# Optimization experiments

Hardware: AMD Instinct MI355X
Metric: run time of the kernel (lower is better)

The kernel has to match this reference:

```python
import jax, jax.numpy as jnp
import numpy as np

ROPE_BASE = 10000.0

def _rope_cos_sin(seq_len, head_dim, dtype):
    half = head_dim // 2
    inv_freq = 1.0 / (ROPE_BASE ** (jnp.arange(0, half, dtype=jnp.float32) / half))
    ang = jnp.arange(seq_len, dtype=jnp.float32)[:, None] * inv_freq[None, :]  # [S, half]
    ang = jnp.concatenate([ang, ang], axis=-1)  # [S, D]
    return jnp.cos(ang).astype(dtype), jnp.sin(ang).astype(dtype)

def _rotate_half(t):
    d = t.shape[-1] // 2
    return jnp.concatenate([-t[..., d:], t[..., :d]], axis=-1)

def _apply_rope(t, cos, sin):
    # t: [B, H, S, D]; cos/sin: [S, D]
    return t * cos[None, None, :, :] + _rotate_half(t) * sin[None, None, :, :]

def setup_inputs() -> dict:
    key = jax.random.key(0)
    ks = jax.random.split(key, 6)
    B, S, DM = 2, 2048, 2048
    x = jax.random.normal(ks[0], (B, S, DM), dtype=jnp.float32)
    attention_mask = jnp.ones((B, S), dtype=jnp.bool_)
    scale = 1.0 / np.sqrt(DM)
    W_in = jax.random.normal(ks[1], (DM, 3 * DM), dtype=jnp.float32) * scale
    b_in = jax.random.normal(ks[2], (3 * DM,), dtype=jnp.float32) * 0.02
    W_out = jax.random.normal(ks[3], (DM, DM), dtype=jnp.float32) * scale
    b_out = jax.random.normal(ks[4], (DM,), dtype=jnp.float32) * 0.02
    return {"x": x, "attention_mask": attention_mask, "W_in": W_in,
            "b_in": b_in, "W_out": W_out, "b_out": b_out}

def reference(x, attention_mask, W_in, b_in, W_out, b_out):
    B, S, DM = x.shape
    H = 16
    D = DM // H
    qkv = x @ W_in + b_in                         # [B, S, 3*DM]
    q, k, v = jnp.split(qkv, 3, axis=-1)
    def to_heads(t):
        return t.reshape(B, S, H, D).transpose(0, 2, 1, 3)  # [B, H, S, D]
    q, k, v = to_heads(q), to_heads(k), to_heads(v)
    cos, sin = _rope_cos_sin(S, D, x.dtype)
    q = _apply_rope(q, cos, sin)
    k = _apply_rope(k, cos, sin)
    scale = 1.0 / np.sqrt(D).astype(np.float32)
    scores = jnp.einsum('bhqd,bhkd->bhqk', q, k) * scale   # [B, H, S, S]
    # SDPA bool mask semantics: True = attend, False = mask out
    mask = attention_mask[:, None, None, :]
    scores = jnp.where(mask, scores, jnp.finfo(scores.dtype).min)
    attn = jax.nn.softmax(scores, axis=-1)
    out = jnp.einsum('bhqk,bhkd->bhqd', attn, v)           # [B, H, S, D]
    out = out.transpose(0, 2, 1, 3).reshape(B, S, DM)
    return out @ W_out + b_out
```

## Files before the change

### kernel.cpp

```cpp
#include <hip/hip_runtime.h>
#include <math.h>

typedef _Float16 f16;
typedef _Float16 f16x4 __attribute__((ext_vector_type(4)));
typedef _Float16 f16x8 __attribute__((ext_vector_type(8)));
typedef float    f32x4 __attribute__((ext_vector_type(4)));

__device__ __forceinline__ void lds_async16(void* lds, const void* g) {
  __builtin_amdgcn_global_load_lds(
      (const __attribute__((address_space(1))) void*)g,
      (__attribute__((address_space(3))) void*)lds, 16, 0, 0);
}

__device__ __forceinline__ f16x4 shfl8(f16x4 v, int srcLane) {
  union { f16x4 h; int i[2]; } u;
  u.h = v;
  u.i[0] = __shfl(u.i[0], srcLane, 64);
  u.i[1] = __shfl(u.i[1], srcLane, 64);
  return u.h;
}

#define BARRIER_FENCE() do { __builtin_amdgcn_s_barrier(); asm volatile("" ::: "memory"); } while (0)
#define WAIT_LGKM0()    asm volatile("s_waitcnt lgkmcnt(0)" ::: "memory")


__global__ __launch_bounds__(256) void f2h4_kernel(const float* __restrict__ in,
                                                   f16* __restrict__ out, int n4) {
  int i = blockIdx.x * 256 + threadIdx.x;
  if (i < n4) {
    float4 v = ((const float4*)in)[i];
    f16x4 h;
    h.x = (f16)v.x; h.y = (f16)v.y; h.z = (f16)v.z; h.w = (f16)v.w;
    ((f16x4*)out)[i] = h;
  }
}

__global__ __launch_bounds__(256) void transpose_f2h(const float* __restrict__ in,
                                                     f16* __restrict__ out,
                                                     int rows, int cols) {
  __shared__ f16 t[64][65];
  int r0 = blockIdx.x * 64, c0 = blockIdx.y * 64;
  int tid = threadIdx.x;
#pragma unroll
  for (int i = 0; i < 16; ++i) {
    int idx = i * 256 + tid;
    int r = idx >> 6, c = idx & 63;
    t[r][c] = (f16)in[(size_t)(r0 + r) * cols + c0 + c];
  }
  __syncthreads();
#pragma unroll
  for (int i = 0; i < 16; ++i) {
    int idx = i * 256 + tid;
    int c = idx >> 6, r = idx & 63;
    out[(size_t)(c0 + c) * rows + r0 + r] = t[r][c];
  }
}

__global__ __launch_bounds__(256) void rope_table_k(float* __restrict__ cosT,
                                                    float* __restrict__ sinT) {
  int idx = blockIdx.x * 256 + threadIdx.x;
  int s = idx >> 6, j = idx & 63;
  double invf = pow(10000.0, -(double)j / 64.0);
  double a = fmod((double)s * invf, 6.283185307179586476925287);
  cosT[s * 64 + j] = (float)cos(a);
  sinT[s * 64 + j] = (float)sin(a);
}

__global__ __launch_bounds__(512, 4) void gemm_qkv(const f16* __restrict__ A,
                                                   const f16* __restrict__ Bt,
                                                   const float* __restrict__ bias,
                                                   const float* __restrict__ cosT,
                                                   const float* __restrict__ sinT,
                                                   f16* __restrict__ Qh, f16* __restrict__ Kh,
                                                   f16* __restrict__ Vt) {
  const int Kd = 2048;
  __shared__ __align__(16) f16 smem[32768];
  f16* Asb = smem;
  f16* Bsb = smem + 16384;
  int tid = threadIdx.x;
  int lane = tid & 63, wave = tid >> 6;
  int wm = wave >> 2, wn = wave & 3;
  int l15 = lane & 15, l4 = lane >> 4;
  int bn = blockIdx.x * 128, bm = blockIdx.y * 128;

  auto stageAq = [&](int buf, int kt, int qh) {
    int rl = tid >> 3, gl = tid & 7;
    int row = qh * 32 + (rl & 31) + (rl >> 5) * 64;
    int gg = gl ^ (rl & 7);
    lds_async16(&Asb[buf * 8192 + row * 64 + gl * 8],
                A + (size_t)(bm + row) * Kd + kt * 64 + gg * 8);
  };
  auto stageBh = [&](int buf, int kt, int h) {
    int rl = tid >> 3, gl = tid & 7;
    int row = h * 64 + rl;
    int gg = gl ^ (rl & 7);
    lds_async16(&Bsb[buf * 8192 + row * 64 + gl * 8],
                Bt + (size_t)(bn + row) * Kd + kt * 64 + gg * 8);
  };

  f32x4 acc[4][2] = {};

  stageAq(0, 0, 0); stageAq(0, 0, 1); stageBh(0, 0, 0); stageBh(0, 0, 1);
  stageAq(1, 1, 0); stageBh(1, 1, 0);
  asm volatile("s_waitcnt vmcnt(2)" ::: "memory");
  BARRIER_FENCE();

  for (int t = 0; t < 32; ++t) {
    int cb = t & 1;
    const f16* as = Asb + cb * 8192;
    const f16* bs = Bsb + cb * 8192;
    f16x8 af[2], bf[2];

#pragma unroll
    for (int j = 0; j < 2; ++j)
      af[j] = *(const f16x8*)&as[(wm * 64 + j * 16 + l15) * 64 + ((l4 ^ (l15 & 7)) * 8)];
#pragma unroll
    for (int nf = 0; nf < 2; ++nf)
      bf[nf] = *(const f16x8*)&bs[((wn + nf * 4) * 16 + l15) * 64 + ((l4 ^ (l15 & 7)) * 8)];
    if (t + 1 < 32) { stageAq(cb ^ 1, t + 1, 1); stageBh(cb ^ 1, t + 1, 1); }
    BARRIER_FENCE();
    WAIT_LGKM0();
    __builtin_amdgcn_s_setprio(1);
#pragma unroll
    for (int j = 0; j < 2; ++j)
#pragma unroll
      for (int nf = 0; nf < 2; ++nf)
        acc[j][nf] = __builtin_amdgcn_mfma_f32_16x16x32_f16(af[j], bf[nf], acc[j][nf], 0, 0, 0);
    __builtin_amdgcn_s_setprio(0);
    BARRIER_FENCE();

#pragma unroll
    for (int j = 0; j < 2; ++j)
      af[j] = *(const f16x8*)&as[(wm * 64 + (2 + j) * 16 + l15) * 64 + ((l4 ^ (l15 & 7)) * 8)];
    BARRIER_FENCE();
    WAIT_LGKM0();
    __builtin_amdgcn_s_setprio(1);
#pragma unroll
    for (int j = 0; j < 2; ++j)
#pragma unroll
      for (int nf = 0; nf < 2; ++nf)
        acc[2 + j][nf] = __builtin_amdgcn_mfma_f32_16x16x32_f16(af[j], bf[nf], acc[2 + j][nf], 0, 0, 0);
    __builtin_amdgcn_s_setprio(0);
    BARRIER_FENCE();

#pragma unroll
    for (int j = 0; j < 2; ++j)
      af[j] = *(const f16x8*)&as[(wm * 64 + j * 16 + l15) * 64 + (((4 + l4) ^ (l15 & 7)) * 8)];
#pragma unroll
    for (int nf = 0; nf < 2; ++nf)
      bf[nf] = *(const f16x8*)&bs[((wn + nf * 4) * 16 + l15) * 64 + (((4 + l4) ^ (l15 & 7)) * 8)];
    BARRIER_FENCE();
    WAIT_LGKM0();
    __builtin_amdgcn_s_setprio(1);
#pragma unroll
    for (int j = 0; j < 2; ++j)
#pragma unroll
      for (int nf = 0; nf < 2; ++nf)
        acc[j][nf] = __builtin_amdgcn_mfma_f32_16x16x32_f16(af[j], bf[nf], acc[j][nf], 0, 0, 0);
    __builtin_amdgcn_s_setprio(0);
    BARRIER_FENCE();

#pragma unroll
    for (int j = 0; j < 2; ++j)
      af[j] = *(const f16x8*)&as[(wm * 64 + (2 + j) * 16 + l15) * 64 + (((4 + l4) ^ (l15 & 7)) * 8)];
    if (t + 2 < 32) { stageBh(cb, t + 2, 0); stageAq(cb, t + 2, 0); }
    BARRIER_FENCE();
    WAIT_LGKM0();
    __builtin_amdgcn_s_setprio(1);
#pragma unroll
    for (int j = 0; j < 2; ++j)
#pragma unroll
      for (int nf = 0; nf < 2; ++nf)
        acc[2 + j][nf] = __builtin_amdgcn_mfma_f32_16x16x32_f16(af[j], bf[nf], acc[2 + j][nf], 0, 0, 0);
    __builtin_amdgcn_s_setprio(0);
    if (t < 30) asm volatile("s_waitcnt vmcnt(2)" ::: "memory");
    else        asm volatile("s_waitcnt vmcnt(0)" ::: "memory");
    BARRIER_FENCE();
  }

  int which = bn >> 11;
  int head  = (bn & 2047) >> 7;
  if (which < 2) {
    f16* dst = which == 0 ? Qh : Kh;
    const float qsc = which == 0 ? 0.08838834764831845f : 1.0f;
    int dlo = wn * 16 + l15;
#pragma unroll
    for (int mi = 0; mi < 4; ++mi)
#pragma unroll
      for (int r = 0; r < 4; ++r) {
        int gm = bm + wm * 64 + mi * 16 + l4 * 4 + r;
        int b = gm >> 11, s = gm & 2047;
        size_t rowbase = ((size_t)(b * 16 + head) * 2048 + s) << 7;
        float cth = cosT[s * 64 + dlo], sth = sinT[s * 64 + dlo];
        float lo = acc[mi][0][r] + bias[bn + dlo];
        float hi = acc[mi][1][r] + bias[bn + dlo + 64];
        dst[rowbase + dlo]      = (f16)((lo * cth - hi * sth) * qsc);
        dst[rowbase + dlo + 64] = (f16)((hi * cth + lo * sth) * qsc);
      }
  } else {
    __syncthreads();
    f16* Vsc = smem;
#pragma unroll
    for (int mi = 0; mi < 4; ++mi)
#pragma unroll
      for (int nf = 0; nf < 2; ++nf) {
        int d = (wn + nf * 4) * 16 + l15;
        int s = wm * 64 + mi * 16 + l4 * 4;
        f16x4 v;
#pragma unroll
        for (int r = 0; r < 4; ++r) v[r] = (f16)(acc[mi][nf][r] + bias[bn + d]);
        int off = d * 128 + ((((s >> 3) ^ ((d & 7) << 1))) << 3) + (s & 7);
        *(f16x4*)&Vsc[off] = v;
      }
    __syncthreads();
    int bm2 = bm & 2047, b = bm >> 11;
#pragma unroll
    for (int it = 0; it < 4; ++it) {
      int idx = it * 512 + tid;
      int d = idx >> 4, gs = idx & 15;
      f16x8 v = *(const f16x8*)&Vsc[d * 128 + ((gs ^ ((d & 7) << 1)) << 3)];
      *(f16x8*)&Vt[((size_t)(b * 16 + head) * 128 + d) * 2048 + bm2 + gs * 8] = v;
    }
  }
}

__global__ __launch_bounds__(512, 4) void gemm_out(const f16* __restrict__ A,
                                                   const f16* __restrict__ Bt,
                                                   const float* __restrict__ bias,
                                                   float* __restrict__ C) {
  const int Kd = 2048, Nd = 2048;
  __shared__ __align__(16) f16 smem[32768];
  f16* Asb = smem;
  f16* Bsb = smem + 16384;
  int tid = threadIdx.x;
  int lane = tid & 63, wave = tid >> 6;
  int wm = wave >> 2, wn = wave & 3;
  int l15 = lane & 15, l4 = lane >> 4;
  int bm = blockIdx.x * 128, bn = blockIdx.y * 128;

  auto stageAq = [&](int buf, int kt, int qh) {
    int rl = tid >> 3, gl = tid & 7;
    int row = qh * 32 + (rl & 31) + (rl >> 5) * 64;
    int gg = gl ^ (rl & 7);
    lds_async16(&Asb[buf * 8192 + row * 64 + gl * 8],
                A + (size_t)(bm + row) * Kd + kt * 64 + gg * 8);
  };
  auto stageBh = [&](int buf, int kt, int h) {
    int rl = tid >> 3, gl = tid & 7;
    int row = h * 64 + rl;
    int gg = gl ^ (rl & 7);
    lds_async16(&Bsb[buf * 8192 + row * 64 + gl * 8],
                Bt + (size_t)(bn + row) * Kd + kt * 64 + gg * 8);
  };

  f32x4 acc[4][2] = {};

  stageAq(0, 0, 0); stageAq(0, 0, 1); stageBh(0, 0, 0); stageBh(0, 0, 1);
  stageAq(1, 1, 0); stageBh(1, 1, 0);
  asm volatile("s_waitcnt vmcnt(2)" ::: "memory");
  BARRIER_FENCE();

  for (int t = 0; t < 32; ++t) {
    int cb = t & 1;
    const f16* as = Asb + cb * 8192;
    const f16* bs = Bsb + cb * 8192;
    f16x8 af[2], bf[2];

#pragma unroll
    for (int j = 0; j < 2; ++j)
      af[j] = *(const f16x8*)&as[(wm * 64 + j * 16 + l15) * 64 + ((l4 ^ (l15 & 7)) * 8)];
#pragma unroll
    for (int nf = 0; nf < 2; ++nf)
      bf[nf] = *(const f16x8*)&bs[(wn * 32 + nf * 16 + l15) * 64 + ((l4 ^ (l15 & 7)) * 8)];
    if (t + 1 < 32) { stageAq(cb ^ 1, t + 1, 1); stageBh(cb ^ 1, t + 1, 1); }
    BARRIER_FENCE();
    WAIT_LGKM0();
    __builtin_amdgcn_s_setprio(1);
#pragma unroll
    for (int j = 0; j < 2; ++j)
#pragma unroll
      for (int nf = 0; nf < 2; ++nf)
        acc[j][nf] = __builtin_amdgcn_mfma_f32_16x16x32_f16(af[j], bf[nf], acc[j][nf], 0, 0, 0);
    __builtin_amdgcn_s_setprio(0);
    BARRIER_FENCE();

#pragma unroll
    for (int j = 0; j < 2; ++j)
      af[j] = *(const f16x8*)&as[(wm * 64 + (2 + j) * 16 + l15) * 64 + ((l4 ^ (l15 & 7)) * 8)];
    BARRIER_FENCE();
    WAIT_LGKM0();
    __builtin_amdgcn_s_setprio(1);
#pragma unroll
    for (int j = 0; j < 2; ++j)
#pragma unroll
      for (int nf = 0; nf < 2; ++nf)
        acc[2 + j][nf] = __builtin_amdgcn_mfma_f32_16x16x32_f16(af[j], bf[nf], acc[2 + j][nf], 0, 0, 0);
    __builtin_amdgcn_s_setprio(0);
    BARRIER_FENCE();

#pragma unroll
    for (int j = 0; j < 2; ++j)
      af[j] = *(const f16x8*)&as[(wm * 64 + j * 16 + l15) * 64 + (((4 + l4) ^ (l15 & 7)) * 8)];
#pragma unroll
    for (int nf = 0; nf < 2; ++nf)
      bf[nf] = *(const f16x8*)&bs[(wn * 32 + nf * 16 + l15) * 64 + (((4 + l4) ^ (l15 & 7)) * 8)];
    BARRIER_FENCE();
    WAIT_LGKM0();
    __builtin_amdgcn_s_setprio(1);
#pragma unroll
    for (int j = 0; j < 2; ++j)
#pragma unroll
      for (int nf = 0; nf < 2; ++nf)
        acc[j][nf] = __builtin_amdgcn_mfma_f32_16x16x32_f16(af[j], bf[nf], acc[j][nf], 0, 0, 0);
    __builtin_amdgcn_s_setprio(0);
    BARRIER_FENCE();

#pragma unroll
    for (int j = 0; j < 2; ++j)
      af[j] = *(const f16x8*)&as[(wm * 64 + (2 + j) * 16 + l15) * 64 + (((4 + l4) ^ (l15 & 7)) * 8)];
    if (t + 2 < 32) { stageBh(cb, t + 2, 0); stageAq(cb, t + 2, 0); }
    BARRIER_FENCE();
    WAIT_LGKM0();
    __builtin_amdgcn_s_setprio(1);
#pragma unroll
    for (int j = 0; j < 2; ++j)
#pragma unroll
      for (int nf = 0; nf < 2; ++nf)
        acc[2 + j][nf] = __builtin_amdgcn_mfma_f32_16x16x32_f16(af[j], bf[nf], acc[2 + j][nf], 0, 0, 0);
    __builtin_amdgcn_s_setprio(0);
    if (t < 30) asm volatile("s_waitcnt vmcnt(2)" ::: "memory");
    else        asm volatile("s_waitcnt vmcnt(0)" ::: "memory");
    BARRIER_FENCE();
  }

#pragma unroll
  for (int mi = 0; mi < 4; ++mi)
#pragma unroll
    for (int nf = 0; nf < 2; ++nf)
#pragma unroll
      for (int r = 0; r < 4; ++r) {
        int gm = bm + wm * 64 + mi * 16 + l4 * 4 + r;
        int gn = bn + wn * 32 + nf * 16 + l15;
        C[(size_t)gm * Nd + gn] = acc[mi][nf][r] + bias[gn];
      }
}

__global__ __launch_bounds__(256, 2) void attn_fwd(const f16* __restrict__ Qh,
                                                   const f16* __restrict__ Kh,
                                                   const f16* __restrict__ Vt,
                                                   f16* __restrict__ O) {
  __shared__ f16 Ks[2][64 * 128];
  __shared__ f16 Vs[2][128 * 64];
  int tid = threadIdx.x, lane = tid & 63, wave = tid >> 6;
  int l15 = lane & 15, l4 = lane >> 4;
  int qt = blockIdx.x, bh = blockIdx.y;
  size_t head = (size_t)bh * (2048 * 128);

  f16x8 qf[2][4];
#pragma unroll
  for (int g = 0; g < 2; ++g) {
    const f16* qrow = Qh + head + (size_t)(qt * 128 + wave * 32 + g * 16 + l15) * 128;
#pragma unroll
    for (int ks = 0; ks < 4; ++ks) qf[g][ks] = *(const f16x8*)(qrow + ks * 32 + l4 * 8);
  }

  auto stage = [&](int buf, int kt) {
#pragma unroll
    for (int i = 0; i < 4; ++i) {
      int c = i * 256 + tid;
      int r = c >> 4, gl = c & 15, gg = gl ^ (r & 15);
      lds_async16(&Ks[buf][c * 8], Kh + head + (size_t)(kt * 64 + r) * 128 + gg * 8);
    }
#pragma unroll
    for (int i = 0; i < 4; ++i) {
      int c = i * 256 + tid;
      int r = c >> 3, gl = c & 7, gg = gl ^ (r & 7);
      lds_async16(&Vs[buf][c * 8], Vt + head + (size_t)r * 2048 + kt * 64 + gg * 8);
    }
  };

  f32x4 acc_o[2][8] = {};
  float m_i[2] = {-1e30f, -1e30f}, l_i[2] = {0.f, 0.f};
  int srcLo = 32 * (l4 & 1) + l15;
  int sel = l4 >> 1;

  stage(0, 0);
  for (int kt = 0; kt < 32; ++kt) {
    int cur = kt & 1;
    __syncthreads();
    if (kt < 31) stage(cur ^ 1, kt + 1);

    f32x4 accs[2][4] = {};
#pragma unroll
    for (int ks = 0; ks < 4; ++ks) {
#pragma unroll
      for (int ms = 0; ms < 4; ++ms) {
        int row = ms * 16 + l15;
        int gl = (ks * 4 + l4) ^ l15;
        f16x8 a = *(const f16x8*)&Ks[cur][row * 128 + gl * 8];
        accs[0][ms] = __builtin_amdgcn_mfma_f32_16x16x32_f16(a, qf[0][ks], accs[0][ms], 0, 0, 0);
        accs[1][ms] = __builtin_amdgcn_mfma_f32_16x16x32_f16(a, qf[1][ks], accs[1][ms], 0, 0, 0);
      }
    }
    f16x8 afrag[2][2];
#pragma unroll
    for (int g = 0; g < 2; ++g) {
      float mx = -1e30f;
#pragma unroll
      for (int ms = 0; ms < 4; ++ms)
#pragma unroll
        for (int r = 0; r < 4; ++r) mx = fmaxf(mx, accs[g][ms][r]);
      mx = fmaxf(mx, __shfl_xor(mx, 16));
      mx = fmaxf(mx, __shfl_xor(mx, 32));
      bool skip = __all(mx - m_i[g] <= 8.0f);
      float mnew, alpha;
      if (skip) {
        mnew = m_i[g];
      } else {
        mnew = fmaxf(m_i[g], mx);
        alpha = __expf(m_i[g] - mnew);
        m_i[g] = mnew;
      }
      float rsum = 0.f;
      f16x4 pv4[4];
#pragma unroll
      for (int ms = 0; ms < 4; ++ms) {
#pragma unroll
        for (int r = 0; r < 4; ++r) {
          float p = __expf(accs[g][ms][r] - mnew);
          rsum += p;
          pv4[ms][r] = (f16)p;
        }
      }
      rsum += __shfl_xor(rsum, 16);
      rsum += __shfl_xor(rsum, 32);
      if (skip) {
        l_i[g] += rsum;
      } else {
        float al[4];
#pragma unroll
        for (int r = 0; r < 4; ++r) al[r] = __shfl(alpha, l4 * 4 + r);
#pragma unroll
        for (int ns = 0; ns < 8; ++ns)
#pragma unroll
          for (int r = 0; r < 4; ++r) acc_o[g][ns][r] *= al[r];
        l_i[g] = l_i[g] * alpha + rsum;
      }
#pragma unroll
      for (int ks = 0; ks < 2; ++ks) {
        f16x4 a0 = shfl8(pv4[2 * ks],     srcLo);
        f16x4 b0 = shfl8(pv4[2 * ks + 1], srcLo);
        f16x4 a1 = shfl8(pv4[2 * ks],     srcLo + 16);
        f16x4 b1 = shfl8(pv4[2 * ks + 1], srcLo + 16);
        f16x4 lo, hi;
        if (sel) { lo = b0; hi = b1; } else { lo = a0; hi = a1; }
        afrag[g][ks][0] = lo[0]; afrag[g][ks][1] = lo[1]; afrag[g][ks][2] = lo[2]; afrag[g][ks][3] = lo[3];
        afrag[g][ks][4] = hi[0]; afrag[g][ks][5] = hi[1]; afrag[g][ks][6] = hi[2]; afrag[g][ks][7] = hi[3];
      }
    }
#pragma unroll
    for (int ks = 0; ks < 2; ++ks) {
#pragma unroll
      for (int ns = 0; ns < 8; ++ns) {
        int row = ns * 16 + l15;
        int gl = (ks * 4 + l4) ^ (l15 & 7);
        f16x8 b = *(const f16x8*)&Vs[cur][row * 64 + gl * 8];
        acc_o[0][ns] = __builtin_amdgcn_mfma_f32_16x16x32_f16(afrag[0][ks], b, acc_o[0][ns], 0, 0, 0);
        acc_o[1][ns] = __builtin_amdgcn_mfma_f32_16x16x32_f16(afrag[1][ks], b, acc_o[1][ns], 0, 0, 0);
      }
    }
  }
  int b = bh >> 4, h = bh & 15;
#pragma unroll
  for (int g = 0; g < 2; ++g) {
    float inv[4];
#pragma unroll
    for (int r = 0; r < 4; ++r) inv[r] = 1.0f / __shfl(l_i[g], l4 * 4 + r);
#pragma unroll
    for (int ns = 0; ns < 8; ++ns)
#pragma unroll
      for (int r = 0; r < 4; ++r) {
        int q = qt * 128 + wave * 32 + g * 16 + l4 * 4 + r;
        int col = h * 128 + ns * 16 + l15;
        O[((size_t)(b * 2048 + q)) * 2048 + col] = (f16)(acc_o[g][ns][r] * inv[r]);
      }
  }
}


extern "C" void kernel_launch(void* const* d_in, const int* in_sizes, int n_in,
                              void* d_out, int out_size, void* d_ws, size_t ws_size,
                              hipStream_t stream) {
  const float* x     = (const float*)d_in[0];
  const float* W_in  = (const float*)d_in[2];
  const float* b_in  = (const float*)d_in[3];
  const float* W_out = (const float*)d_in[4];
  const float* b_out = (const float*)d_in[5];
  float* out = (float*)d_out;

  char* w = (char*)d_ws;
  f16*   Xh    = (f16*)(w);
  f16*   WinT  = (f16*)(w + 16777216ull);
  f16*   WoutT = (f16*)(w + 41943040ull);
  float* cosT  = (float*)(w + 50331648ull);
  float* sinT  = (float*)(w + 51380224ull);
  f16*   Qh    = (f16*)(w + 52428800ull);
  f16*   Kh    = (f16*)(w + 69206016ull);
  f16*   A2    = (f16*)(w + 85983232ull);
  f16*   Vt    = (f16*)(w + 102760448ull);

  f2h4_kernel<<<dim3(8192), dim3(256), 0, stream>>>(x, Xh, 8388608 / 4);
  transpose_f2h<<<dim3(32, 96), dim3(256), 0, stream>>>(W_in, WinT, 2048, 6144);
  transpose_f2h<<<dim3(32, 32), dim3(256), 0, stream>>>(W_out, WoutT, 2048, 2048);
  rope_table_k<<<dim3(512), dim3(256), 0, stream>>>(cosT, sinT);
  gemm_qkv<<<dim3(48, 32), dim3(512), 0, stream>>>(Xh, WinT, b_in, cosT, sinT, Qh, Kh, Vt);
  attn_fwd<<<dim3(16, 32), dim3(256), 0, stream>>>(Qh, Kh, Vt, A2);
  gemm_out<<<dim3(32, 16), dim3(512), 0, stream>>>(A2, WoutT, b_out, out);
}
```

Measured before the change: 395.8 us.

## Single-buffer V in attention for higher occupancy; use 4-wave gemm_out tiles

The attention kernel drops V double-buffering. It loads V for the current tile at the start of each iteration and waits for it just before the PV matmul, which cuts LDS from 64KB to 48KB so launch bounds can allow 3 blocks per CU. The output GEMM moves from 8 waves to 4 waves per block, each computing a 64x64 sub-tile with twice the loads per thread. The trade-off is less overlap of V loading with compute and higher register pressure in gemm_out, in exchange for more resident attention blocks.

New measurement: 425.3 us. 7.4% more time.

```diff
diff --git a/kernel.cpp b/kernel.cpp
--- a/kernel.cpp
+++ b/kernel.cpp
@@ -224,7 +224,7 @@
   }
 }
 
-__global__ __launch_bounds__(512, 4) void gemm_out(const f16* __restrict__ A,
+__global__ __launch_bounds__(256, 2) void gemm_out(const f16* __restrict__ A,
                                                    const f16* __restrict__ Bt,
                                                    const float* __restrict__ bias,
                                                    float* __restrict__ C) {
@@ -234,44 +234,52 @@
   f16* Bsb = smem + 16384;
   int tid = threadIdx.x;
   int lane = tid & 63, wave = tid >> 6;
-  int wm = wave >> 2, wn = wave & 3;
+  int wm = wave >> 1, wn = wave & 1;
   int l15 = lane & 15, l4 = lane >> 4;
   int bm = blockIdx.x * 128, bn = blockIdx.y * 128;
 
   auto stageAq = [&](int buf, int kt, int qh) {
-    int rl = tid >> 3, gl = tid & 7;
-    int row = qh * 32 + (rl & 31) + (rl >> 5) * 64;
-    int gg = gl ^ (rl & 7);
-    lds_async16(&Asb[buf * 8192 + row * 64 + gl * 8],
-                A + (size_t)(bm + row) * Kd + kt * 64 + gg * 8);
+#pragma unroll
+    for (int i = 0; i < 2; ++i) {
+      int c = i * 256 + tid;
+      int rl = c >> 3, gl = c & 7;
+      int row = qh * 32 + (rl & 31) + (rl >> 5) * 64;
+      int gg = gl ^ (rl & 7);
+      lds_async16(&Asb[buf * 8192 + row * 64 + gl * 8],
+                  A + (size_t)(bm + row) * Kd + kt * 64 + gg * 8);
+    }
   };
   auto stageBh = [&](int buf, int kt, int h) {
-    int rl = tid >> 3, gl = tid & 7;
-    int row = h * 64 + rl;
-    int gg = gl ^ (rl & 7);
-    lds_async16(&Bsb[buf * 8192 + row * 64 + gl * 8],
-                Bt + (size_t)(bn + row) * Kd + kt * 64 + gg * 8);
+#pragma unroll
+    for (int i = 0; i < 2; ++i) {
+      int c = i * 256 + tid;
+      int rl = c >> 3, gl = c & 7;
+      int row = h * 64 + rl;
+      int gg = gl ^ (rl & 7);
+      lds_async16(&Bsb[buf * 8192 + row * 64 + gl * 8],
+                  Bt + (size_t)(bn + row) * Kd + kt * 64 + gg * 8);
+    }
   };
 
-  f32x4 acc[4][2] = {};
+  f32x4 acc[4][4] = {};
 
   stageAq(0, 0, 0); stageAq(0, 0, 1); stageBh(0, 0, 0); stageBh(0, 0, 1);
   stageAq(1, 1, 0); stageBh(1, 1, 0);
-  asm volatile("s_waitcnt vmcnt(2)" ::: "memory");
+  asm volatile("s_waitcnt vmcnt(4)" ::: "memory");
   BARRIER_FENCE();
 
   for (int t = 0; t < 32; ++t) {
     int cb = t & 1;
     const f16* as = Asb + cb * 8192;
     const f16* bs = Bsb + cb * 8192;
-    f16x8 af[2], bf[2];
+    f16x8 af[2], bf[4];
 
 #pragma unroll
     for (int j = 0; j < 2; ++j)
       af[j] = *(const f16x8*)&as[(wm * 64 + j * 16 + l15) * 64 + ((l4 ^ (l15 & 7)) * 8)];
 #pragma unroll
-    for (int nf = 0; nf < 2; ++nf)
-      bf[nf] = *(const f16x8*)&bs[(wn * 32 + nf * 16 + l15) * 64 + ((l4 ^ (l15 & 7)) * 8)];
+    for (int nf = 0; nf < 4; ++nf)
+      bf[nf] = *(const f16x8*)&bs[(wn * 64 + nf * 16 + l15) * 64 + ((l4 ^ (l15 & 7)) * 8)];
     if (t + 1 < 32) { stageAq(cb ^ 1, t + 1, 1); stageBh(cb ^ 1, t + 1, 1); }
     BARRIER_FENCE();
     WAIT_LGKM0();
@@ -279,7 +287,7 @@
 #pragma unroll
     for (int j = 0; j < 2; ++j)
 #pragma unroll
-      for (int nf = 0; nf < 2; ++nf)
+      for (int nf = 0; nf < 4; ++nf)
         acc[j][nf] = __builtin_amdgcn_mfma_f32_16x16x32_f16(af[j], bf[nf], acc[j][nf], 0, 0, 0);
     __builtin_amdgcn_s_setprio(0);
     BARRIER_FENCE();
@@ -293,7 +301,7 @@
 #pragma unroll
     for (int j = 0; j < 2; ++j)
 #pragma unroll
-      for (int nf = 0; nf < 2; ++nf)
+      for (int nf = 0; nf < 4; ++nf)
         acc[2 + j][nf] = __builtin_amdgcn_mfma_f32_16x16x32_f16(af[j], bf[nf], acc[2 + j][nf], 0, 0, 0);
     __builtin_amdgcn_s_setprio(0);
     BARRIER_FENCE();
@@ -302,15 +310,15 @@
     for (int j = 0; j < 2; ++j)
       af[j] = *(const f16x8*)&as[(wm * 64 + j * 16 + l15) * 64 + (((4 + l4) ^ (l15 & 7)) * 8)];
 #pragma unroll
-    for (int nf = 0; nf < 2; ++nf)
-      bf[nf] = *(const f16x8*)&bs[(wn * 32 + nf * 16 + l15) * 64 + (((4 + l4) ^ (l15 & 7)) * 8)];
-    BARRIER_FENCE();
-    WAIT_LGKM0();
-    __builtin_amdgcn_s_setprio(1);
-#pragma unroll
-    for (int j = 0; j < 2; ++j)
-#pragma unroll
-      for (int nf = 0; nf < 2; ++nf)
+    for (int nf = 0; nf < 4; ++nf)
+      bf[nf] = *(const f16x8*)&bs[(wn * 64 + nf * 16 + l15) * 64 + (((4 + l4) ^ (l15 & 7)) * 8)];
+    BARRIER_FENCE();
+    WAIT_LGKM0();
+    __builtin_amdgcn_s_setprio(1);
+#pragma unroll
+    for (int j = 0; j < 2; ++j)
+#pragma unroll
+      for (int nf = 0; nf < 4; ++nf)
         acc[j][nf] = __builtin_amdgcn_mfma_f32_16x16x32_f16(af[j], bf[nf], acc[j][nf], 0, 0, 0);
     __builtin_amdgcn_s_setprio(0);
     BARRIER_FENCE();
@@ -325,10 +333,10 @@
 #pragma unroll
     for (int j = 0; j < 2; ++j)
 #pragma unroll
-      for (int nf = 0; nf < 2; ++nf)
+      for (int nf = 0; nf < 4; ++nf)
         acc[2 + j][nf] = __builtin_amdgcn_mfma_f32_16x16x32_f16(af[j], bf[nf], acc[2 + j][nf], 0, 0, 0);
     __builtin_amdgcn_s_setprio(0);
-    if (t < 30) asm volatile("s_waitcnt vmcnt(2)" ::: "memory");
+    if (t < 30) asm volatile("s_waitcnt vmcnt(4)" ::: "memory");
     else        asm volatile("s_waitcnt vmcnt(0)" ::: "memory");
     BARRIER_FENCE();
   }
@@ -336,21 +344,21 @@
 #pragma unroll
   for (int mi = 0; mi < 4; ++mi)
 #pragma unroll
-    for (int nf = 0; nf < 2; ++nf)
+    for (int nf = 0; nf < 4; ++nf)
 #pragma unroll
       for (int r = 0; r < 4; ++r) {
         int gm = bm + wm * 64 + mi * 16 + l4 * 4 + r;
-        int gn = bn + wn * 32 + nf * 16 + l15;
+        int gn = bn + wn * 64 + nf * 16 + l15;
         C[(size_t)gm * Nd + gn] = acc[mi][nf][r] + bias[gn];
       }
 }
 
-__global__ __launch_bounds__(256, 2) void attn_fwd(const f16* __restrict__ Qh,
+__global__ __launch_bounds__(256, 3) void attn_fwd(const f16* __restrict__ Qh,
                                                    const f16* __restrict__ Kh,
                                                    const f16* __restrict__ Vt,
                                                    f16* __restrict__ O) {
   __shared__ f16 Ks[2][64 * 128];
-  __shared__ f16 Vs[2][128 * 64];
+  __shared__ f16 Vs[128 * 64];
   int tid = threadIdx.x, lane = tid & 63, wave = tid >> 6;
   int l15 = lane & 15, l4 = lane >> 4;
   int qt = blockIdx.x, bh = blockIdx.y;
@@ -364,18 +372,20 @@
     for (int ks = 0; ks < 4; ++ks) qf[g][ks] = *(const f16x8*)(qrow + ks * 32 + l4 * 8);
   }
 
-  auto stage = [&](int buf, int kt) {
+  auto stageK = [&](int buf, int kt) {
 #pragma unroll
     for (int i = 0; i < 4; ++i) {
       int c = i * 256 + tid;
       int r = c >> 4, gl = c & 15, gg = gl ^ (r & 15);
       lds_async16(&Ks[buf][c * 8], Kh + head + (size_t)(kt * 64 + r) * 128 + gg * 8);
     }
+  };
+  auto stageV = [&](int kt) {
 #pragma unroll
     for (int i = 0; i < 4; ++i) {
       int c = i * 256 + tid;
       int r = c >> 3, gl = c & 7, gg = gl ^ (r & 7);
-      lds_async16(&Vs[buf][c * 8], Vt + head + (size_t)r * 2048 + kt * 64 + gg * 8);
+      lds_async16(&Vs[c * 8], Vt + head + (size_t)r * 2048 + kt * 64 + gg * 8);
     }
   };
 
@@ -384,11 +394,13 @@
   int srcLo = 32 * (l4 & 1) + l15;
   int sel = l4 >> 1;
 
-  stage(0, 0);
+  stageK(0, 0);
   for (int kt = 0; kt < 32; ++kt) {
     int cur = kt & 1;
-    __syncthreads();
-    if (kt < 31) stage(cur ^ 1, kt + 1);
+    asm volatile("s_waitcnt vmcnt(0)" ::: "memory");
+    BARRIER_FENCE();
+    stageV(kt);
+    if (kt < 31) stageK(cur ^ 1, kt + 1);
 
     f32x4 accs[2][4] = {};
 #pragma unroll
@@ -458,13 +470,16 @@
         afrag[g][ks][4] = hi[0]; afrag[g][ks][5] = hi[1]; afrag[g][ks][6] = hi[2]; afrag[g][ks][7] = hi[3];
       }
     }
+    if (kt < 31) asm volatile("s_waitcnt vmcnt(4)" ::: "memory");
+    else         asm volatile("s_waitcnt vmcnt(0)" ::: "memory");
+    BARRIER_FENCE();
 #pragma unroll
     for (int ks = 0; ks < 2; ++ks) {
 #pragma unroll
       for (int ns = 0; ns < 8; ++ns) {
         int row = ns * 16 + l15;
         int gl = (ks * 4 + l4) ^ (l15 & 7);
-        f16x8 b = *(const f16x8*)&Vs[cur][row * 64 + gl * 8];
+        f16x8 b = *(const f16x8*)&Vs[row * 64 + gl * 8];
         acc_o[0][ns] = __builtin_amdgcn_mfma_f32_16x16x32_f16(afrag[0][ks], b, acc_o[0][ns], 0, 0, 0);
         acc_o[1][ns] = __builtin_amdgcn_mfma_f32_16x16x32_f16(afrag[1][ks], b, acc_o[1][ns], 0, 0, 0);
       }
@@ -515,5 +530,5 @@
   rope_table_k<<<dim3(512), dim3(256), 0, stream>>>(cosT, sinT);
   gemm_qkv<<<dim3(48, 32), dim3(512), 0, stream>>>(Xh, WinT, b_in, cosT, sinT, Qh, Kh, Vt);
   attn_fwd<<<dim3(16, 32), dim3(256), 0, stream>>>(Qh, Kh, Vt, A2);
-  gemm_out<<<dim3(32, 16), dim3(512), 0, stream>>>(A2, WoutT, b_out, out);
-}
+  gemm_out<<<dim3(32, 16), dim3(256), 0, stream>>>(A2, WoutT, b_out, out);
+}
```
